# Kernel tuning notes

Hardware: AMD Instinct MI355X
Metric: run time of the kernel (lower is better)

Reference implementation:

```python
import jax, jax.numpy as jnp
import numpy as np

N, CS, CZ, H, C, PQ, PV, N0, N1 = 768, 384, 128, 12, 64, 4, 8, 192, 64
CZ4 = CZ // 4
INF, EPS = 1e5, 1e-8


def setup_inputs() -> dict:
    key = jax.random.key(0)
    ks = jax.random.split(key, 24)

    def w(k, i, o):
        return jax.random.normal(k, (i, o), jnp.float32) / np.float32(np.sqrt(i))

    s = jax.random.normal(ks[0], (N, CS), jnp.float32)
    z = jax.random.normal(ks[1], (N, N, CZ), jnp.float32)
    rot = jnp.linalg.qr(jax.random.normal(ks[2], (N, 3, 3), jnp.float32))[0]
    trans = jax.random.normal(ks[3], (N, 3), jnp.float32)
    mask = jnp.ones((N,), jnp.float32)
    is_atom = jax.random.bernoulli(ks[4], 0.5, (N,))
    return dict(
        s=s, z=z, rot=rot, trans=trans, mask=mask, is_atom=is_atom,
        wq=w(ks[5], CS, H * C), bq=jnp.zeros((H * C,), jnp.float32),
        wkv=w(ks[6], CS, 2 * H * C), bkv=jnp.zeros((2 * H * C,), jnp.float32),
        wqp=w(ks[7], CS, 3 * H * PQ), bqp=jnp.zeros((3 * H * PQ,), jnp.float32),
        wkvp=w(ks[8], CS, 3 * H * (PQ + PV)), bkvp=jnp.zeros((3 * H * (PQ + PV),), jnp.float32),
        wb=w(ks[9], CZ, H), bb=jnp.zeros((H,), jnp.float32),
        wdz=w(ks[10], CZ, CZ4), bdz=jnp.zeros((CZ4,), jnp.float32),
        head_weights=jnp.full((H,), 0.5413248, jnp.float32),  # softplus^-1(1), per ipa_point_weights_init_
        wout=w(ks[11], H * (C + 4 * PV + CZ4), CS), bout=jnp.zeros((CS,), jnp.float32),
        tfnq_ws=w(ks[12], N0, H * C), tfnq_wv=w(ks[13], N1, H * PQ),
        tfnkv_ws=w(ks[14], N0, 2 * H * C), tfnkv_wv=w(ks[15], N1, H * (PQ + PV)),
        tfno_ws=w(ks[16], H * (C + PV + CZ4), N0), tfno_wv=w(ks[17], H * PV, N1),
    )


def reference(s, z, rot, trans, mask, is_atom, wq, bq, wkv, bkv, wqp, bqp, wkvp, bkvp,
              wb, bb, wdz, bdz, head_weights, wout, bout,
              tfnq_ws, tfnq_wv, tfnkv_ws, tfnkv_wv, tfno_ws, tfno_wv):
    n = s.shape[0]

    def apply_rigid(pts):  # pts: [n, P, 3] -> R x + t
        return jnp.einsum('nij,npj->npi', rot, pts) + trans[:, None, :]

    # ---- residue (frame) path ----
    q_r = (s @ wq + bq).reshape(n, H, C)
    kv_r = (s @ wkv + bkv).reshape(n, H, 2 * C)
    k_r, v_r = kv_r[..., :C], kv_r[..., C:]
    # torch.split-in-3 then stack(dim=-1) layout: [n, 3, H*P] -> [n, H*P, 3]
    qp = (s @ wqp + bqp).reshape(n, 3, H * PQ).transpose(0, 2, 1)
    q_pts_r = apply_rigid(qp).reshape(n, H, PQ, 3)
    kvp = (s @ wkvp + bkvp).reshape(n, 3, H * (PQ + PV)).transpose(0, 2, 1)
    kv_pts_r = apply_rigid(kvp).reshape(n, H, PQ + PV, 3)
    k_pts_r, v_pts_r = kv_pts_r[..., :PQ, :], kv_pts_r[..., PQ:, :]

    # ---- atom (TFN-equivariant) path: irreps = N0 scalars + N1 vectors ----
    sc = s[:, :N0]
    vec = s[:, N0:N0 + 3 * N1].reshape(n, N1, 3)
    q_a = (sc @ tfnq_ws).reshape(n, H, C)
    q_pts_a = jnp.einsum('nix,io->nox', vec, tfnq_wv).reshape(n, H, PQ, 3) + trans[:, None, None, :]
    kv_a = (sc @ tfnkv_ws).reshape(n, H, 2 * C)
    k_a, v_a = kv_a[..., :C], kv_a[..., C:]
    kv_pts_a = jnp.einsum('nix,io->nox', vec, tfnkv_wv).reshape(n, H, PQ + PV, 3) + trans[:, None, None, :]
    k_pts_a, v_pts_a = kv_pts_a[..., :PQ, :], kv_pts_a[..., PQ:, :]

    m1 = is_atom[:, None, None]
    m2 = is_atom[:, None, None, None]
    q = jnp.where(m1, q_a, q_r)
    k = jnp.where(m1, k_a, k_r)
    v = jnp.where(m1, v_a, v_r)
    q_pts = jnp.where(m2, q_pts_a, q_pts_r)
    k_pts = jnp.where(m2, k_pts_a, k_pts_r)
    v_pts = jnp.where(m2, v_pts_a, v_pts_r)

    # ---- attention logits ----
    b = z @ wb + bb  # [n, n, H]
    a = jnp.einsum('nhc,mhc->hnm', q, k) * np.float32(np.sqrt(1.0 / (3 * C)))
    a = a + np.float32(np.sqrt(1.0 / 3)) * b.transpose(2, 0, 1)

    disp = q_pts[:, None] - k_pts[None]          # [n, n, H, PQ, 3]
    pt_att = jnp.sum(disp * disp, axis=-1)       # [n, n, H, PQ]
    hw = jax.nn.softplus(head_weights) * np.float32(np.sqrt(1.0 / (3 * (PQ * 9.0 / 2))))
    pt_att = -0.5 * jnp.sum(pt_att * hw[:, None], axis=-1)  # [n, n, H]
    a = a + pt_att.transpose(2, 0, 1)

    sq_mask = INF * (mask[:, None] * mask[None, :] - 1.0)
    a = jax.nn.softmax(a + sq_mask[None], axis=-1)  # [H, n, n]

    # ---- aggregation ----
    o = jnp.einsum('hnm,mhc->nhc', a, v).reshape(n, H * C)
    o_pt = jnp.einsum('hnm,mhpx->nhpx', a, v_pts)  # [n, H, PV, 3]
    o_pt = jnp.einsum('nji,nhpj->nhpi', rot, o_pt - trans[:, None, None, :])  # invert_apply
    o_pt_norm = jnp.sqrt(jnp.sum(o_pt * o_pt, axis=-1) + EPS).reshape(n, H * PV)
    o_pt = o_pt.reshape(n, H * PV, 3)
    pair_z = z @ wdz + bdz  # [n, n, CZ4]
    o_pair = jnp.einsum('hnm,nmz->nhz', a, pair_z).reshape(n, H * CZ4)

    # ---- residue output head ----
    res_feats = jnp.concatenate([o, o_pt[..., 0], o_pt[..., 1], o_pt[..., 2], o_pt_norm, o_pair], axis=-1)
    res_out = res_feats @ wout + bout  # [n, CS]

    # ---- atom output head (equivariant linear: scalars mix, vectors mix per-component) ----
    atom_sc = jnp.concatenate([o, o_pt_norm, o_pair], axis=-1) @ tfno_ws  # [n, N0]
    atom_vec = jnp.einsum('npx,po->nox', o_pt, tfno_wv).reshape(n, 3 * N1)
    atom_out = jnp.concatenate([atom_sc, atom_vec], axis=-1)  # [n, CS]

    return jnp.where(is_atom[:, None], atom_out, res_out)
```

## Files before the change

### kernel.cpp

```cpp
#include <hip/hip_runtime.h>
#include <hip/hip_bf16.h>

static constexpr int NN = 768;

typedef short v8bf __attribute__((ext_vector_type(8)));
typedef float v4f  __attribute__((ext_vector_type(4)));

__device__ __forceinline__ unsigned short f2bf(float f) {
  unsigned u = __float_as_uint(f);
  u += 0x7fffu + ((u >> 16) & 1u);
  return (unsigned short)(u >> 16);
}
__device__ __forceinline__ float bf2f(unsigned short s) {
  return __uint_as_float(((unsigned)s) << 16);
}

static constexpr size_t OFF_ISA    = 0;
static constexpr size_t OFF_WCT    = 1024;
static constexpr size_t OFF_BCAT   = 4096;
static constexpr size_t OFF_SBF    = 4160;
static constexpr size_t OFF_WQT    = 151616;
static constexpr size_t OFF_WKVT   = 299072;
static constexpr size_t OFF_WQPT   = 593984;
static constexpr size_t OFF_WKVPT  = 630848;
static constexpr size_t OFF_TFNQT  = 716864;
static constexpr size_t OFF_TFNKVT = 815168;
static constexpr size_t OFF_WOUTT  = 1011776;
static constexpr size_t OFF_TFNOT  = 1306688;
static constexpr size_t OFF_QR     = 1429568;
static constexpr size_t OFF_KVR    = 1724480;
static constexpr size_t OFF_QP     = 2314304;
static constexpr size_t OFF_KVP    = 2424896;
static constexpr size_t OFF_QA     = 2756672;
static constexpr size_t OFF_KVA    = 3051584;
static constexpr size_t OFF_QCAT   = 3641408;
static constexpr size_t OFF_KCAT   = 4083776;
static constexpr size_t OFF_RQ     = 4526144;
static constexpr size_t OFF_RK     = 4535360;
static constexpr size_t OFF_VCATT  = 4986944;
static constexpr size_t OFF_BB     = 5429312;
static constexpr size_t OFF_PZT    = 8968256;
static constexpr size_t OFF_ABF    = 18405440;
static constexpr size_t OFF_OPTRAW = 21944384;
static constexpr size_t OFF_RESF   = 22165568;
static constexpr size_t OFF_ATOMF  = 22755392;

__device__ void transpose_cv(const float* __restrict__ src, unsigned short* __restrict__ dst,
                             int K, int Kp, int N, int ky, int nx) {
  __shared__ float tl[32][33];
  const int k0 = ky * 32, n0 = nx * 32;
  const int tx = threadIdx.x & 31, ty = threadIdx.x >> 5;
  for (int it = 0; it < 4; ++it) {
    int r = ty + it * 8;
    float v = 0.f;
    if (k0 + r < K && n0 + tx < N) v = src[(long long)(k0 + r) * N + n0 + tx];
    tl[r][tx] = v;
  }
  __syncthreads();
  for (int it = 0; it < 4; ++it) {
    int r = ty + it * 8;
    if (n0 + r < N && k0 + tx < Kp)
      dst[(long long)(n0 + r) * Kp + k0 + tx] = f2bf(tl[tx][r]);
  }
}

__global__ __launch_bounds__(256) void prep0(
    float* wsf, const float* s, const float* wq, const float* wkv,
    const float* wqp, const float* wkvp, const float* tfnq_ws,
    const float* tfnkv_ws, const float* wout, const float* tfno_ws,
    const float* wb, const float* wdz, const float* bb, const float* bdz,
    const unsigned int* isa_raw)
{
  const int bx = blockIdx.x, t = threadIdx.x;
  if (bx < 288)       { int g = bx;        transpose_cv(wq,      (unsigned short*)(wsf+OFF_WQT),    384, 384, 768,  g/24, g%24); return; }
  else if (bx < 864)  { int g = bx-288;    transpose_cv(wkv,     (unsigned short*)(wsf+OFF_WKVT),   384, 384, 1536, g/48, g%48); return; }
  else if (bx < 924)  { int g = bx-864;    transpose_cv(wqp,     (unsigned short*)(wsf+OFF_WQPT),   384, 384, 144,  g/5,  g%5);  return; }
  else if (bx < 1092) { int g = bx-924;    transpose_cv(wkvp,    (unsigned short*)(wsf+OFF_WKVPT),  384, 384, 432,  g/14, g%14); return; }
  else if (bx < 1284) { int g = bx-1092;   transpose_cv(tfnq_ws, (unsigned short*)(wsf+OFF_TFNQT),  192, 256, 768,  g/24, g%24); return; }
  else if (bx < 1668) { int g = bx-1284;   transpose_cv(tfnkv_ws,(unsigned short*)(wsf+OFF_TFNKVT), 192, 256, 1536, g/48, g%48); return; }
  else if (bx < 2244) { int g = bx-1668;   transpose_cv(wout,    (unsigned short*)(wsf+OFF_WOUTT),  1536,1536,384,  g/12, g%12); return; }
  else if (bx < 2484) { int g = bx-2244;   transpose_cv(tfno_ws, (unsigned short*)(wsf+OFF_TFNOT),  1248,1280,192,  g/6,  g%6);  return; }
  else if (bx < 2772) {
    long long base = (long long)(bx - 2484) * 1024 + t * 4;
    float4 v = *(const float4*)(s + base);
    unsigned short tmp[4] = {f2bf(v.x), f2bf(v.y), f2bf(v.z), f2bf(v.w)};
    *(uint2*)((unsigned short*)(wsf + OFF_SBF) + base) = *(uint2*)tmp;
    return;
  } else if (bx < 2773) {
    __shared__ int notint, notfloat;
    int* ISA = (int*)(wsf + OFF_ISA);
    if (t == 0) { notint = 0; notfloat = 0; }
    __syncthreads();
    if (t < 192) {
      unsigned v = isa_raw[t];
      if (v > 1u) atomicOr(&notint, 1);
      if (v != 0u && v != 0x3F800000u) atomicOr(&notfloat, 1);
    }
    __syncthreads();
    const int mode = (!notint) ? 0 : ((!notfloat) ? 1 : 2);
    for (int n = t; n < NN; n += 256) {
      int val;
      if (mode == 2) val = (((const unsigned char*)isa_raw)[n] != 0);
      else           val = (isa_raw[n] != 0u);
      ISA[n] = val;
    }
    return;
  } else {
    const float rs3 = 0.57735026918962576f;
    unsigned short* WCT = (unsigned short*)(wsf + OFF_WCT);
    float* bcat = wsf + OFF_BCAT;
    int idx = (bx - 2773) * 256 + t;
    if (idx < 48 * 128) {
      int o = idx >> 7, k = idx & 127;
      float v = 0.f;
      if (o < 12) v = rs3 * wb[k * 12 + o];
      else if (o < 44) v = wdz[k * 32 + (o - 12)];
      WCT[o * 128 + k] = f2bf(v);
    }
    if (bx == 2773 && t < 48)
      bcat[t] = (t < 12) ? rs3 * bb[t] : (t < 44 ? bdz[t - 12] : 0.f);
  }
}

__device__ __forceinline__ void gemm16(
    char* lds, const unsigned short* __restrict__ A, int lda,
    const unsigned short* __restrict__ BT, int ldb, int KQ,
    const float* __restrict__ bias, int mode,
    float* Cf, unsigned short* Cb, int ldc, int Nc, int colb, int row0,
    const int* __restrict__ ISA, float* outp)
{
  v4f (*PS)[4][64] = (v4f (*)[4][64])lds;
  const int t = threadIdx.x, w = t >> 6, l = t & 63, l15 = l & 15, lg = l >> 4;
  const int rowA = row0 + l15;
  v4f acc[4] = {};
  const unsigned short* ap = A + (long long)rowA * lda + lg * 8;
  const int kend = (w + 1) * KQ;
  for (int k0 = w * KQ; k0 < kend; k0 += 32) {
    v8bf av = *(const v8bf*)(ap + k0);
#pragma unroll
    for (int cf = 0; cf < 4; ++cf) {
      v8bf bv = *(const v8bf*)(BT + (long long)(colb + cf * 16 + l15) * ldb + k0 + lg * 8);
      acc[cf] = __builtin_amdgcn_mfma_f32_16x16x32_bf16(av, bv, acc[cf], 0, 0, 0);
    }
  }
#pragma unroll
  for (int cf = 0; cf < 4; ++cf) PS[w][cf][l] = acc[cf];
  __syncthreads();
  const int cf = w;
  v4f sv = PS[0][cf][l] + PS[1][cf][l] + PS[2][cf][l] + PS[3][cf][l];
  const int c = colb + cf * 16 + l15;
  if (c < Nc) {
    float bvs = bias ? bias[c] : 0.f;
#pragma unroll
    for (int i = 0; i < 4; ++i) {
      int r = row0 + lg * 4 + i;
      float v = sv[i] + bvs;
      if (mode == 0)      Cf[(long long)r * ldc + c] = v;
      else if (mode == 1) Cb[(long long)r * ldc + c] = f2bf(v);
      else if (mode == 2) { if (!ISA[r]) outp[r * 384 + c] = v; }
      else                { if ( ISA[r]) outp[r * 384 + c] = v; }
    }
  }
}

__global__ __launch_bounds__(256) void mega1(
    float* wsf, const float* __restrict__ z,
    const float* bq, const float* bkv, const float* bqp, const float* bkvp)
{
  __shared__ __align__(16) char lds[23296];
  const int t = threadIdx.x;
  if (blockIdx.x < 4608) {
    float* Sout = (float*)lds;
    const unsigned short* WCT = (const unsigned short*)(wsf + OFF_WCT);
    const float* bcat = wsf + OFF_BCAT;
    unsigned short* Bb  = (unsigned short*)(wsf + OFF_BB);
    unsigned short* PZT = (unsigned short*)(wsf + OFF_PZT);
    const long long row0 = (long long)blockIdx.x * 128;
    const int w = t >> 6, l = t & 63, l15 = l & 15, lg = l >> 4;
    v8bf bvv[4][3];
#pragma unroll
    for (int ks = 0; ks < 4; ++ks)
#pragma unroll
      for (int cf = 0; cf < 3; ++cf)
        bvv[ks][cf] = *(const v8bf*)(WCT + (cf * 16 + l15) * 128 + ks * 32 + lg * 8);
    v4f acc[2][3] = {};
#pragma unroll
    for (int rf = 0; rf < 2; ++rf) {
      const float* zrow = z + (row0 + w * 32 + rf * 16 + l15) * 128 + lg * 8;
#pragma unroll
      for (int ks = 0; ks < 4; ++ks) {
        float4 a0 = *(const float4*)(zrow + ks * 32);
        float4 a1 = *(const float4*)(zrow + ks * 32 + 4);
        unsigned short tmp[8] = {f2bf(a0.x), f2bf(a0.y), f2bf(a0.z), f2bf(a0.w),
                                 f2bf(a1.x), f2bf(a1.y), f2bf(a1.z), f2bf(a1.w)};
        v8bf av = *(const v8bf*)tmp;
#pragma unroll
        for (int cf = 0; cf < 3; ++cf)
          acc[rf][cf] = __builtin_amdgcn_mfma_f32_16x16x32_bf16(av, bvv[ks][cf], acc[rf][cf], 0, 0, 0);
      }
    }
#pragma unroll
    for (int rf = 0; rf < 2; ++rf)
#pragma unroll
      for (int cf = 0; cf < 3; ++cf) {
        int o = cf * 16 + l15;
#pragma unroll
        for (int i = 0; i < 4; ++i) {
          int m = w * 32 + rf * 16 + lg * 4 + i;
          Sout[o * 132 + m] = acc[rf][cf][i];
        }
      }
    __syncthreads();
    const int n = blockIdx.x / 6;
    const int m0 = (blockIdx.x % 6) * 128;
    for (int idx = t; idx < 44 * 8; idx += 256) {
      int o = idx >> 3, seg = idx & 7;
      float bias = bcat[o];
      unsigned short tmp[16];
#pragma unroll
      for (int j = 0; j < 16; ++j) tmp[j] = f2bf(Sout[o * 132 + seg * 16 + j] + bias);
      unsigned short* gp;
      if (o < 12) gp = Bb + ((long long)o * 768 + n) * 768 + m0 + seg * 16;
      else        gp = PZT + ((long long)n * 32 + (o - 12)) * 768 + m0 + seg * 16;
      *(uint4*)gp = *(uint4*)tmp;
      *(uint4*)(gp + 8) = *(uint4*)(tmp + 8);
    }
    return;
  }
  const int g = blockIdx.x - 4608;
  const int bt = g / 82, xt = g % 82;
  const unsigned short* SBF = (const unsigned short*)(wsf + OFF_SBF);
  const unsigned short* BT; const float* bias; int ldb, KQ, mode, ldc, Nc, colb;
  float* Cf = nullptr; unsigned short* Cb = nullptr;
  if (xt < 12)      { BT=(const unsigned short*)(wsf+OFF_WQT);    bias=bq;     ldb=384; KQ=96; Cb=(unsigned short*)(wsf+OFF_QR);  ldc=768;  Nc=768;  colb=xt*64;      mode=1; }
  else if (xt < 36) { BT=(const unsigned short*)(wsf+OFF_WKVT);   bias=bkv;    ldb=384; KQ=96; Cb=(unsigned short*)(wsf+OFF_KVR); ldc=1536; Nc=1536; colb=(xt-12)*64; mode=1; }
  else if (xt < 39) { BT=(const unsigned short*)(wsf+OFF_WQPT);   bias=bqp;    ldb=384; KQ=96; Cf=wsf+OFF_QP;                     ldc=144;  Nc=144;  colb=(xt-36)*64; mode=0; }
  else if (xt < 46) { BT=(const unsigned short*)(wsf+OFF_WKVPT);  bias=bkvp;   ldb=384; KQ=96; Cf=wsf+OFF_KVP;                    ldc=432;  Nc=432;  colb=(xt-39)*64; mode=0; }
  else if (xt < 58) { BT=(const unsigned short*)(wsf+OFF_TFNQT);  bias=nullptr;ldb=256; KQ=64; Cb=(unsigned short*)(wsf+OFF_QA);  ldc=768;  Nc=768;  colb=(xt-46)*64; mode=1; }
  else              { BT=(const unsigned short*)(wsf+OFF_TFNKVT); bias=nullptr;ldb=256; KQ=64; Cb=(unsigned short*)(wsf+OFF_KVA); ldc=1536; Nc=1536; colb=(xt-58)*64; mode=1; }
  gemm16(lds, SBF, 384, BT, ldb, KQ, bias, mode, Cf, Cb, ldc, Nc, colb, bt * 16, nullptr, nullptr);
}

__global__ __launch_bounds__(256) void prep_qkv(
    float* wsf, const float* __restrict__ s,
    const float* __restrict__ rot, const float* __restrict__ trans,
    const float* __restrict__ head_w,
    const float* __restrict__ tfnq_wv, const float* __restrict__ tfnkv_wv)
{
  const int n = blockIdx.x, t = threadIdx.x;
  const int* ISA = (const int*)(wsf + OFF_ISA);
  const unsigned short* QRb  = (const unsigned short*)(wsf + OFF_QR);
  const unsigned short* KVRb = (const unsigned short*)(wsf + OFF_KVR);
  const unsigned short* QAb  = (const unsigned short*)(wsf + OFF_QA);
  const unsigned short* KVAb = (const unsigned short*)(wsf + OFF_KVA);
  const float* QP  = wsf + OFF_QP;
  const float* KVP = wsf + OFF_KVP;
  unsigned short* Qcat = (unsigned short*)(wsf + OFF_QCAT);
  unsigned short* Kcat = (unsigned short*)(wsf + OFF_KCAT);
  unsigned short* Vt   = (unsigned short*)(wsf + OFF_VCATT);
  float* rq = wsf + OFF_RQ;
  float* rk = wsf + OFF_RK;
  const bool isa = ISA[n] != 0;
  __shared__ float R[9], T[3], shw[12], sv[192];
  __shared__ float qs[768], ks[768], vs[768], qp[144], kp[144], vp[288];
  if (t < 9) R[t] = rot[n * 9 + t];
  if (t < 3) T[t] = trans[n * 3 + t];
  if (t >= 16 && t < 28)
    shw[t - 16] = log1pf(__expf(head_w[t - 16])) * 0.13608276348795434f;
  if (isa && t >= 32 && t < 224) sv[t - 32] = s[(size_t)n * 384 + 192 + (t - 32)];
  __syncthreads();
  for (int idx = t; idx < 768; idx += 256) {
    int h = idx >> 6, c = idx & 63;
    qs[idx] = bf2f(isa ? QAb[(long long)n * 768 + idx] : QRb[(long long)n * 768 + idx]);
    ks[idx] = bf2f(isa ? KVAb[(long long)n * 1536 + h * 128 + c] : KVRb[(long long)n * 1536 + h * 128 + c]);
    vs[idx] = bf2f(isa ? KVAb[(long long)n * 1536 + h * 128 + 64 + c] : KVRb[(long long)n * 1536 + h * 128 + 64 + c]);
  }
  if (isa) {
    for (int idx = t; idx < 144; idx += 256) {
      int hp = idx / 3, x = idx % 3;
      float a = 0.f;
      for (int i = 0; i < 64; ++i) a += sv[i * 3 + x] * tfnq_wv[i * 48 + hp];
      qp[idx] = a + T[x];
    }
    for (int idx = t; idx < 432; idx += 256) {
      int o = idx / 3, x = idx % 3;
      float a = 0.f;
      for (int i = 0; i < 64; ++i) a += sv[i * 3 + x] * tfnkv_wv[i * 144 + o];
      float v = a + T[x];
      int h = o / 12, pp = o % 12;
      if (pp < 4) kp[(h * 4 + pp) * 3 + x] = v;
      else        vp[(h * 8 + (pp - 4)) * 3 + x] = v;
    }
  } else {
    for (int idx = t; idx < 144; idx += 256) {
      int hp = idx / 3, i = idx % 3;
      qp[idx] = R[i * 3 + 0] * QP[(long long)n * 144 + 0 + hp] +
                R[i * 3 + 1] * QP[(long long)n * 144 + 48 + hp] +
                R[i * 3 + 2] * QP[(long long)n * 144 + 96 + hp] + T[i];
    }
    for (int idx = t; idx < 432; idx += 256) {
      int hp = idx / 3, i = idx % 3;
      float v = R[i * 3 + 0] * KVP[(long long)n * 432 + 0 + hp] +
                R[i * 3 + 1] * KVP[(long long)n * 432 + 144 + hp] +
                R[i * 3 + 2] * KVP[(long long)n * 432 + 288 + hp] + T[i];
      int h = hp / 12, pp = hp % 12;
      if (pp < 4) kp[(h * 4 + pp) * 3 + i] = v;
      else        vp[(h * 8 + (pp - 4)) * 3 + i] = v;
    }
  }
  __syncthreads();
  const float sq = 0.07216878364870322f;
  for (int idx = t; idx < 1152; idx += 256) {
    int h = idx / 96, c = idx % 96;
    float qv = (c < 64) ? sq * qs[h * 64 + c] : ((c < 76) ? shw[h] * qp[h * 12 + (c - 64)] : 0.f);
    float kv = (c < 64) ? ks[h * 64 + c]      : ((c < 76) ? kp[h * 12 + (c - 64)] : 0.f);
    float vv = (c < 64) ? vs[h * 64 + c]      : ((c < 88) ? vp[h * 24 + (c - 64)] : 0.f);
    long long base = ((long long)n * 12 + h) * 96 + c;
    Qcat[base] = f2bf(qv);
    Kcat[base] = f2bf(kv);
    Vt[((long long)h * 96 + c) * 768 + n] = f2bf(vv);
  }
  if (t < 24) {
    int h = t >> 1, which = t & 1;
    const float* p = which ? kp : qp;
    float s2 = 0.f;
#pragma unroll
    for (int d = 0; d < 12; ++d) { float x = p[h * 12 + d]; s2 += x * x; }
    float val = 0.5f * shw[h] * s2;
    if (which) rk[h * 768 + n] = val;
    else       rq[h * 768 + n] = val;
  }
}

__global__ __launch_bounds__(256) void mega2(float* wsf, const float* __restrict__ mask) {
  __shared__ __align__(16) char lds[26112];
  const int t = threadIdx.x;
  const unsigned short* Qcat = (const unsigned short*)(wsf + OFF_QCAT);
  const unsigned short* Kcat = (const unsigned short*)(wsf + OFF_KCAT);
  const unsigned short* Bb   = (const unsigned short*)(wsf + OFF_BB);
  const unsigned short* VcatT= (const unsigned short*)(wsf + OFF_VCATT);
  const float* rq = wsf + OFF_RQ;
  const float* rk = wsf + OFF_RK;
  unsigned short* Abf   = (unsigned short*)(wsf + OFF_ABF);
  unsigned short* RESF  = (unsigned short*)(wsf + OFF_RESF);
  unsigned short* ATOMF = (unsigned short*)(wsf + OFF_ATOMF);
  float* OPTRAW = wsf + OFF_OPTRAW;
  const int h = blockIdx.x / 48, r0 = (blockIdx.x % 48) * 16;
  const int w = t >> 6, l = t & 63, l15 = l & 15, lg = l >> 4;
  unsigned short* SW = (unsigned short*)lds + w * 3200;
  float* redm = (float*)(lds + 25600);
  float* reds = (float*)(lds + 25856);
  const int nrow = r0 + l15;
  v8bf aq[3];
#pragma unroll
  for (int ks = 0; ks < 3; ++ks)
    aq[ks] = *(const v8bf*)(Qcat + ((long long)nrow * 12 + h) * 96 + ks * 32 + lg * 8);
  v4f acc[12] = {};
#pragma unroll
  for (int cf = 0; cf < 12; ++cf) {
    int m = w * 192 + cf * 16 + l15;
    const unsigned short* kb = Kcat + ((long long)m * 12 + h) * 96 + lg * 8;
#pragma unroll
    for (int ks = 0; ks < 3; ++ks) {
      v8bf bv = *(const v8bf*)(kb + ks * 32);
      acc[cf] = __builtin_amdgcn_mfma_f32_16x16x32_bf16(aq[ks], bv, acc[cf], 0, 0, 0);
    }
  }
#pragma unroll
  for (int it = 0; it < 6; ++it) {
    int chunk = it * 64 + l;
    int row = chunk / 24, cc = (chunk % 24) * 8;
    *(uint4*)(SW + row * 200 + cc) =
        *(const uint4*)(Bb + ((long long)(h * 768 + r0 + row)) * 768 + w * 192 + cc);
  }
  __syncthreads();
  float rkm[12], mkm[12];
#pragma unroll
  for (int cf = 0; cf < 12; ++cf) {
    int m = w * 192 + cf * 16 + l15;
    rkm[cf] = rk[h * 768 + m];
    mkm[cf] = mask[m];
  }
  float rqn[4], mkn[4], mymax[4];
#pragma unroll
  for (int i = 0; i < 4; ++i) {
    int gn = r0 + lg * 4 + i;
    rqn[i] = rq[h * 768 + gn];
    mkn[i] = mask[gn];
    mymax[i] = -3.0e38f;
  }
#pragma unroll
  for (int cf = 0; cf < 12; ++cf)
#pragma unroll
    for (int i = 0; i < 4; ++i) {
      float v = acc[cf][i] + bf2f(SW[(lg * 4 + i) * 200 + cf * 16 + l15])
              - rqn[i] - rkm[cf] + 100000.0f * (mkn[i] * mkm[cf] - 1.0f);
      acc[cf][i] = v;
      mymax[i] = fmaxf(mymax[i], v);
    }
#pragma unroll
  for (int off = 1; off < 16; off <<= 1)
#pragma unroll
    for (int i = 0; i < 4; ++i) mymax[i] = fmaxf(mymax[i], __shfl_xor(mymax[i], off, 64));
  if (l15 == 0) {
#pragma unroll
    for (int i = 0; i < 4; ++i) redm[w * 16 + lg * 4 + i] = mymax[i];
  }
  __syncthreads();
  float mx[4], mysum[4];
#pragma unroll
  for (int i = 0; i < 4; ++i) {
    int rl = lg * 4 + i;
    mx[i] = fmaxf(fmaxf(redm[rl], redm[16 + rl]), fmaxf(redm[32 + rl], redm[48 + rl]));
    mysum[i] = 0.f;
  }
#pragma unroll
  for (int cf = 0; cf < 12; ++cf)
#pragma unroll
    for (int i = 0; i < 4; ++i) {
      float e = __expf(acc[cf][i] - mx[i]);
      acc[cf][i] = e;
      mysum[i] += e;
    }
#pragma unroll
  for (int off = 1; off < 16; off <<= 1)
#pragma unroll
    for (int i = 0; i < 4; ++i) mysum[i] += __shfl_xor(mysum[i], off, 64);
  if (l15 == 0) {
#pragma unroll
    for (int i = 0; i < 4; ++i) reds[w * 16 + lg * 4 + i] = mysum[i];
  }
  __syncthreads();
  float inv[4];
#pragma unroll
  for (int i = 0; i < 4; ++i) {
    int rl = lg * 4 + i;
    inv[i] = 1.0f / (reds[rl] + reds[16 + rl] + reds[32 + rl] + reds[48 + rl]);
  }
#pragma unroll
  for (int cf = 0; cf < 12; ++cf)
#pragma unroll
    for (int i = 0; i < 4; ++i)
      SW[(lg * 4 + i) * 200 + cf * 16 + l15] = f2bf(acc[cf][i] * inv[i]);
  __syncthreads();
#pragma unroll
  for (int it = 0; it < 6; ++it) {
    int chunk = it * 64 + l;
    int row = chunk / 24, cc = (chunk % 24) * 8;
    *(uint4*)(Abf + ((long long)(h * 768 + r0 + row)) * 768 + w * 192 + cc) =
        *(const uint4*)(SW + row * 200 + cc);
  }
  const unsigned short* vbase = VcatT + (long long)h * 96 * 768 + w * 192 + lg * 8;
  v4f acc2[6] = {};
  for (int kk = 0; kk < 192; kk += 32) {
    v8bf av = *(const v8bf*)(SW + l15 * 200 + kk + lg * 8);
#pragma unroll
    for (int cf = 0; cf < 6; ++cf) {
      v8bf bv = *(const v8bf*)(vbase + (long long)(cf * 16 + l15) * 768 + kk);
      acc2[cf] = __builtin_amdgcn_mfma_f32_16x16x32_bf16(av, bv, acc2[cf], 0, 0, 0);
    }
  }
  __syncthreads();
  v4f (*PS)[64] = (v4f (*)[64])lds;
#pragma unroll
  for (int cf = 0; cf < 6; ++cf) PS[w * 6 + cf][l] = acc2[cf];
  __syncthreads();
  for (int cf = w; cf < 6; cf += 4) {
    v4f sv = PS[cf][l] + PS[6 + cf][l] + PS[12 + cf][l] + PS[18 + cf][l];
    int c = cf * 16 + l15;
    int rb = r0 + lg * 4;
#pragma unroll
    for (int i = 0; i < 4; ++i) {
      int n = rb + i;
      float v = sv[i];
      if (c < 64) {
        unsigned short b = f2bf(v);
        RESF[(long long)n * 1536 + h * 64 + c] = b;
        ATOMF[(long long)n * 1280 + h * 64 + c] = b;
      } else if (c < 88) {
        OPTRAW[(long long)n * 288 + h * 24 + (c - 64)] = v;
      }
    }
  }
}

__global__ __launch_bounds__(256) void mega3(
    float* wsf, const float* __restrict__ rot, const float* __restrict__ trans,
    const float* __restrict__ tfno_wv, float* __restrict__ out)
{
  const int t = threadIdx.x;
  unsigned short* RESF  = (unsigned short*)(wsf + OFF_RESF);
  unsigned short* ATOMF = (unsigned short*)(wsf + OFF_ATOMF);
  if (blockIdx.x < 768) {
    __shared__ __align__(16) v4f PS[8][64];
    const unsigned short* Abf = (const unsigned short*)(wsf + OFF_ABF);
    const unsigned short* PZT = (const unsigned short*)(wsf + OFF_PZT);
    const int w = t >> 6, l = t & 63, l15 = l & 15, lg = l >> 4;
    const int n = blockIdx.x;
    const int hh = (l15 < 12) ? l15 : 0;
    const unsigned short* arow = Abf + ((long long)hh * 768 + n) * 768 + lg * 8;
    const unsigned short* pz = PZT + (long long)n * 32 * 768 + lg * 8;
    v4f acc[2] = {};
    for (int k0 = w * 192; k0 < w * 192 + 192; k0 += 32) {
      v8bf av = *(const v8bf*)(arow + k0);
#pragma unroll
      for (int cf = 0; cf < 2; ++cf) {
        v8bf bv = *(const v8bf*)(pz + (long long)(cf * 16 + l15) * 768 + k0);
        acc[cf] = __builtin_amdgcn_mfma_f32_16x16x32_bf16(av, bv, acc[cf], 0, 0, 0);
      }
    }
    PS[w * 2 + 0][l] = acc[0];
    PS[w * 2 + 1][l] = acc[1];
    __syncthreads();
    if (t < 128) {
      int cf = t >> 6, ll = t & 63;
      v4f sv = PS[cf][ll] + PS[2 + cf][ll] + PS[4 + cf][ll] + PS[6 + cf][ll];
      int zc = cf * 16 + (ll & 15);
#pragma unroll
      for (int i = 0; i < 4; ++i) {
        int hd = (ll >> 4) * 4 + i;
        if (hd < 12) {
          unsigned short b = f2bf(sv[i]);
          RESF[(long long)n * 1536 + 1152 + hd * 32 + zc] = b;
          ATOMF[(long long)n * 1280 + 864 + hd * 32 + zc] = b;
        }
      }
    }
    return;
  }
  {
    const int n = blockIdx.x - 768;
    const float* OPTRAW = wsf + OFF_OPTRAW;
    const int* ISA = (const int*)(wsf + OFF_ISA);
    const bool isa = ISA[n] != 0;
    __shared__ float R[9], T[3], opt2[96][3], norml[96];
    if (t < 9) R[t] = rot[(size_t)n * 9 + t];
    if (t < 3) T[t] = trans[(size_t)n * 3 + t];
    __syncthreads();
    for (int idx = t; idx < 288; idx += 256) {
      int hp = idx / 3, i = idx % 3;
      float x = OPTRAW[(size_t)n * 288 + hp * 3 + 0] - T[0];
      float y = OPTRAW[(size_t)n * 288 + hp * 3 + 1] - T[1];
      float z = OPTRAW[(size_t)n * 288 + hp * 3 + 2] - T[2];
      opt2[hp][i] = R[0 + i] * x + R[3 + i] * y + R[6 + i] * z;
    }
    __syncthreads();
    if (t < 96)
      norml[t] = sqrtf(opt2[t][0] * opt2[t][0] + opt2[t][1] * opt2[t][1] +
                       opt2[t][2] * opt2[t][2] + 1e-8f);
    __syncthreads();
    const long long rb = (long long)n * 1536;
    const long long ab = (long long)n * 1280;
    for (int idx = t; idx < 288; idx += 256) {
      int x = idx / 96, hp = idx % 96;
      RESF[rb + 768 + idx] = f2bf(opt2[hp][x]);
    }
    for (int idx = t; idx < 96; idx += 256) {
      unsigned short b = f2bf(norml[idx]);
      RESF[rb + 1056 + idx] = b;
      ATOMF[ab + 768 + idx] = b;
    }
    if (isa) {
      for (int idx = t; idx < 192; idx += 256) {
        int o = idx / 3, x = idx % 3;
        float a = 0.f;
        for (int p = 0; p < 96; ++p) a += opt2[p][x] * tfno_wv[p * 64 + o];
        out[(size_t)n * 384 + 192 + idx] = a;
      }
    }
  }
}

__global__ __launch_bounds__(256) void outg(float* wsf, const float* __restrict__ bout,
                                            float* __restrict__ out) {
  __shared__ __align__(16) char lds[16384];
  const int g = blockIdx.x;
  const int bt = g / 9, xt = g % 9;
  const int* ISA = (const int*)(wsf + OFF_ISA);
  if (xt < 6)
    gemm16(lds, (const unsigned short*)(wsf + OFF_RESF), 1536,
           (const unsigned short*)(wsf + OFF_WOUTT), 1536, 384, bout, 2,
           nullptr, nullptr, 0, 384, xt * 64, bt * 16, ISA, out);
  else
    gemm16(lds, (const unsigned short*)(wsf + OFF_ATOMF), 1280,
           (const unsigned short*)(wsf + OFF_TFNOT), 1280, 320, nullptr, 3,
           nullptr, nullptr, 0, 192, (xt - 6) * 64, bt * 16, ISA, out);
}

extern "C" void kernel_launch(void* const* d_in, const int* in_sizes, int n_in,
                              void* d_out, int out_size, void* d_ws, size_t ws_size,
                              hipStream_t stream) {
  (void)in_sizes; (void)n_in; (void)out_size; (void)ws_size;
  const float* s      = (const float*)d_in[0];
  const float* z      = (const float*)d_in[1];
  const float* rot    = (const float*)d_in[2];
  const float* trans  = (const float*)d_in[3];
  const float* mask   = (const float*)d_in[4];
  const float* wq     = (const float*)d_in[6];
  const float* bq     = (const float*)d_in[7];
  const float* wkv    = (const float*)d_in[8];
  const float* bkv    = (const float*)d_in[9];
  const float* wqp    = (const float*)d_in[10];
  const float* bqp    = (const float*)d_in[11];
  const float* wkvp   = (const float*)d_in[12];
  const float* bkvp   = (const float*)d_in[13];
  const float* wb     = (const float*)d_in[14];
  const float* bb     = (const float*)d_in[15];
  const float* wdz    = (const float*)d_in[16];
  const float* bdz    = (const float*)d_in[17];
  const float* head_w = (const float*)d_in[18];
  const float* wout   = (const float*)d_in[19];
  const float* bout   = (const float*)d_in[20];
  const float* tfnq_ws  = (const float*)d_in[21];
  const float* tfnq_wv  = (const float*)d_in[22];
  const float* tfnkv_ws = (const float*)d_in[23];
  const float* tfnkv_wv = (const float*)d_in[24];
  const float* tfno_ws  = (const float*)d_in[25];
  const float* tfno_wv  = (const float*)d_in[26];

  float* wsf = (float*)d_ws;

  prep0<<<2797, 256, 0, stream>>>(wsf, s, wq, wkv, wqp, wkvp, tfnq_ws, tfnkv_ws,
                                  wout, tfno_ws, wb, wdz, bb, bdz,
                                  (const unsigned int*)d_in[5]);
  mega1<<<8544, 256, 0, stream>>>(wsf, z, bq, bkv, bqp, bkvp);
  prep_qkv<<<768, 256, 0, stream>>>(wsf, s, rot, trans, head_w, tfnq_wv, tfnkv_wv);
  mega2<<<576, 256, 0, stream>>>(wsf, mask);
  mega3<<<1536, 256, 0, stream>>>(wsf, rot, trans, tfno_wv, (float*)d_out);
  outg<<<432, 256, 0, stream>>>(wsf, bout, (float*)d_out);
}
```

Measured before the change: 186.1 us.

## Widen attention kernel to 8 waves, move output-weight transposes into mega1

The attention kernel mega2 now runs 512 threads per block, with each wave covering 96 key columns instead of 192. This halves the per-wave register accumulators and adds more parallelism, at the cost of twice the LDS and an 8-way cross-wave reduction. The attention-probability buffer is stored in [n][h][m] layout, so mega3 reads the 12 heads for a row from contiguous memory. The wout and tfno_ws transposes move out of prep0 into extra blocks of mega1, shortening the prep kernel and overlapping that work with the z projection.

```diff
diff --git a/kernel.cpp b/kernel.cpp
--- a/kernel.cpp
+++ b/kernel.cpp
@@ -45,11 +45,12 @@
 static constexpr size_t OFF_RESF   = 22165568;
 static constexpr size_t OFF_ATOMF  = 22755392;
 
-__device__ void transpose_cv(const float* __restrict__ src, unsigned short* __restrict__ dst,
+__device__ void transpose_cv(char* ldsbuf, const float* __restrict__ src,
+                             unsigned short* __restrict__ dst,
                              int K, int Kp, int N, int ky, int nx) {
-  __shared__ float tl[32][33];
+  float (*tl)[33] = (float (*)[33])ldsbuf;
   const int k0 = ky * 32, n0 = nx * 32;
-  const int tx = threadIdx.x & 31, ty = threadIdx.x >> 5;
+  const int tx = threadIdx.x & 31, ty = (threadIdx.x & 255) >> 5;
   for (int it = 0; it < 4; ++it) {
     int r = ty + it * 8;
     float v = 0.f;
@@ -67,26 +68,24 @@
 __global__ __launch_bounds__(256) void prep0(
     float* wsf, const float* s, const float* wq, const float* wkv,
     const float* wqp, const float* wkvp, const float* tfnq_ws,
-    const float* tfnkv_ws, const float* wout, const float* tfno_ws,
-    const float* wb, const float* wdz, const float* bb, const float* bdz,
-    const unsigned int* isa_raw)
+    const float* tfnkv_ws, const float* wb, const float* wdz,
+    const float* bb, const float* bdz, const unsigned int* isa_raw)
 {
+  __shared__ __align__(16) char lds[4224];
   const int bx = blockIdx.x, t = threadIdx.x;
-  if (bx < 288)       { int g = bx;        transpose_cv(wq,      (unsigned short*)(wsf+OFF_WQT),    384, 384, 768,  g/24, g%24); return; }
-  else if (bx < 864)  { int g = bx-288;    transpose_cv(wkv,     (unsigned short*)(wsf+OFF_WKVT),   384, 384, 1536, g/48, g%48); return; }
-  else if (bx < 924)  { int g = bx-864;    transpose_cv(wqp,     (unsigned short*)(wsf+OFF_WQPT),   384, 384, 144,  g/5,  g%5);  return; }
-  else if (bx < 1092) { int g = bx-924;    transpose_cv(wkvp,    (unsigned short*)(wsf+OFF_WKVPT),  384, 384, 432,  g/14, g%14); return; }
-  else if (bx < 1284) { int g = bx-1092;   transpose_cv(tfnq_ws, (unsigned short*)(wsf+OFF_TFNQT),  192, 256, 768,  g/24, g%24); return; }
-  else if (bx < 1668) { int g = bx-1284;   transpose_cv(tfnkv_ws,(unsigned short*)(wsf+OFF_TFNKVT), 192, 256, 1536, g/48, g%48); return; }
-  else if (bx < 2244) { int g = bx-1668;   transpose_cv(wout,    (unsigned short*)(wsf+OFF_WOUTT),  1536,1536,384,  g/12, g%12); return; }
-  else if (bx < 2484) { int g = bx-2244;   transpose_cv(tfno_ws, (unsigned short*)(wsf+OFF_TFNOT),  1248,1280,192,  g/6,  g%6);  return; }
-  else if (bx < 2772) {
-    long long base = (long long)(bx - 2484) * 1024 + t * 4;
+  if (bx < 288)       { int g = bx;        transpose_cv(lds, wq,      (unsigned short*)(wsf+OFF_WQT),    384, 384, 768,  g/24, g%24); return; }
+  else if (bx < 864)  { int g = bx-288;    transpose_cv(lds, wkv,     (unsigned short*)(wsf+OFF_WKVT),   384, 384, 1536, g/48, g%48); return; }
+  else if (bx < 924)  { int g = bx-864;    transpose_cv(lds, wqp,     (unsigned short*)(wsf+OFF_WQPT),   384, 384, 144,  g/5,  g%5);  return; }
+  else if (bx < 1092) { int g = bx-924;    transpose_cv(lds, wkvp,    (unsigned short*)(wsf+OFF_WKVPT),  384, 384, 432,  g/14, g%14); return; }
+  else if (bx < 1284) { int g = bx-1092;   transpose_cv(lds, tfnq_ws, (unsigned short*)(wsf+OFF_TFNQT),  192, 256, 768,  g/24, g%24); return; }
+  else if (bx < 1668) { int g = bx-1284;   transpose_cv(lds, tfnkv_ws,(unsigned short*)(wsf+OFF_TFNKVT), 192, 256, 1536, g/48, g%48); return; }
+  else if (bx < 1956) {
+    long long base = (long long)(bx - 1668) * 1024 + t * 4;
     float4 v = *(const float4*)(s + base);
     unsigned short tmp[4] = {f2bf(v.x), f2bf(v.y), f2bf(v.z), f2bf(v.w)};
     *(uint2*)((unsigned short*)(wsf + OFF_SBF) + base) = *(uint2*)tmp;
     return;
-  } else if (bx < 2773) {
+  } else if (bx < 1957) {
     __shared__ int notint, notfloat;
     int* ISA = (int*)(wsf + OFF_ISA);
     if (t == 0) { notint = 0; notfloat = 0; }
@@ -109,7 +108,7 @@
     const float rs3 = 0.57735026918962576f;
     unsigned short* WCT = (unsigned short*)(wsf + OFF_WCT);
     float* bcat = wsf + OFF_BCAT;
-    int idx = (bx - 2773) * 256 + t;
+    int idx = (bx - 1957) * 256 + t;
     if (idx < 48 * 128) {
       int o = idx >> 7, k = idx & 127;
       float v = 0.f;
@@ -117,7 +116,7 @@
       else if (o < 44) v = wdz[k * 32 + (o - 12)];
       WCT[o * 128 + k] = f2bf(v);
     }
-    if (bx == 2773 && t < 48)
+    if (bx == 1957 && t < 48)
       bcat[t] = (t < 12) ? rs3 * bb[t] : (t < 44 ? bdz[t - 12] : 0.f);
   }
 }
@@ -165,7 +164,8 @@
 
 __global__ __launch_bounds__(256) void mega1(
     float* wsf, const float* __restrict__ z,
-    const float* bq, const float* bkv, const float* bqp, const float* bkvp)
+    const float* bq, const float* bkv, const float* bqp, const float* bkvp,
+    const float* wout, const float* tfno_ws)
 {
   __shared__ __align__(16) char lds[23296];
   const int t = threadIdx.x;
@@ -225,6 +225,12 @@
       *(uint4*)gp = *(uint4*)tmp;
       *(uint4*)(gp + 8) = *(uint4*)(tmp + 8);
     }
+    return;
+  }
+  if (blockIdx.x >= 8544) {
+    const int g = blockIdx.x - 8544;
+    if (g < 576) transpose_cv(lds, wout,    (unsigned short*)(wsf+OFF_WOUTT), 1536, 1536, 384, g/12, g%12);
+    else         transpose_cv(lds, tfno_ws, (unsigned short*)(wsf+OFF_TFNOT), 1248, 1280, 192, (g-576)/6, (g-576)%6);
     return;
   }
   const int g = blockIdx.x - 4608;
@@ -332,8 +338,8 @@
   }
 }
 
-__global__ __launch_bounds__(256) void mega2(float* wsf, const float* __restrict__ mask) {
-  __shared__ __align__(16) char lds[26112];
+__global__ __launch_bounds__(512) void mega2(float* wsf, const float* __restrict__ mask) {
+  __shared__ __align__(16) char lds[50176];
   const int t = threadIdx.x;
   const unsigned short* Qcat = (const unsigned short*)(wsf + OFF_QCAT);
   const unsigned short* Kcat = (const unsigned short*)(wsf + OFF_KCAT);
@@ -341,24 +347,24 @@
   const unsigned short* VcatT= (const unsigned short*)(wsf + OFF_VCATT);
   const float* rq = wsf + OFF_RQ;
   const float* rk = wsf + OFF_RK;
-  unsigned short* Abf   = (unsigned short*)(wsf + OFF_ABF);
+  unsigned short* Abf2  = (unsigned short*)(wsf + OFF_ABF);
   unsigned short* RESF  = (unsigned short*)(wsf + OFF_RESF);
   unsigned short* ATOMF = (unsigned short*)(wsf + OFF_ATOMF);
   float* OPTRAW = wsf + OFF_OPTRAW;
   const int h = blockIdx.x / 48, r0 = (blockIdx.x % 48) * 16;
   const int w = t >> 6, l = t & 63, l15 = l & 15, lg = l >> 4;
-  unsigned short* SW = (unsigned short*)lds + w * 3200;
-  float* redm = (float*)(lds + 25600);
-  float* reds = (float*)(lds + 25856);
+  unsigned short* SW = (unsigned short*)(lds + w * 3328);
+  float* redm = (float*)(lds + 49152);
+  float* reds = (float*)(lds + 49664);
   const int nrow = r0 + l15;
   v8bf aq[3];
 #pragma unroll
   for (int ks = 0; ks < 3; ++ks)
     aq[ks] = *(const v8bf*)(Qcat + ((long long)nrow * 12 + h) * 96 + ks * 32 + lg * 8);
-  v4f acc[12] = {};
-#pragma unroll
-  for (int cf = 0; cf < 12; ++cf) {
-    int m = w * 192 + cf * 16 + l15;
+  v4f acc[6] = {};
+#pragma unroll
+  for (int cf = 0; cf < 6; ++cf) {
+    int m = w * 96 + cf * 16 + l15;
     const unsigned short* kb = Kcat + ((long long)m * 12 + h) * 96 + lg * 8;
 #pragma unroll
     for (int ks = 0; ks < 3; ++ks) {
@@ -367,17 +373,17 @@
     }
   }
 #pragma unroll
-  for (int it = 0; it < 6; ++it) {
+  for (int it = 0; it < 3; ++it) {
     int chunk = it * 64 + l;
-    int row = chunk / 24, cc = (chunk % 24) * 8;
-    *(uint4*)(SW + row * 200 + cc) =
-        *(const uint4*)(Bb + ((long long)(h * 768 + r0 + row)) * 768 + w * 192 + cc);
-  }
-  __syncthreads();
-  float rkm[12], mkm[12];
-#pragma unroll
-  for (int cf = 0; cf < 12; ++cf) {
-    int m = w * 192 + cf * 16 + l15;
+    int row = chunk / 12, cc = (chunk % 12) * 8;
+    *(uint4*)(SW + row * 104 + cc) =
+        *(const uint4*)(Bb + ((long long)(h * 768 + r0 + row)) * 768 + w * 96 + cc);
+  }
+  __syncthreads();
+  float rkm[6], mkm[6];
+#pragma unroll
+  for (int cf = 0; cf < 6; ++cf) {
+    int m = w * 96 + cf * 16 + l15;
     rkm[cf] = rk[h * 768 + m];
     mkm[cf] = mask[m];
   }
@@ -390,10 +396,10 @@
     mymax[i] = -3.0e38f;
   }
 #pragma unroll
-  for (int cf = 0; cf < 12; ++cf)
+  for (int cf = 0; cf < 6; ++cf)
 #pragma unroll
     for (int i = 0; i < 4; ++i) {
-      float v = acc[cf][i] + bf2f(SW[(lg * 4 + i) * 200 + cf * 16 + l15])
+      float v = acc[cf][i] + bf2f(SW[(lg * 4 + i) * 104 + cf * 16 + l15])
               - rqn[i] - rkm[cf] + 100000.0f * (mkn[i] * mkm[cf] - 1.0f);
       acc[cf][i] = v;
       mymax[i] = fmaxf(mymax[i], v);
@@ -411,11 +417,15 @@
 #pragma unroll
   for (int i = 0; i < 4; ++i) {
     int rl = lg * 4 + i;
-    mx[i] = fmaxf(fmaxf(redm[rl], redm[16 + rl]), fmaxf(redm[32 + rl], redm[48 + rl]));
+    float m0 = fmaxf(redm[rl], redm[16 + rl]);
+    float m1 = fmaxf(redm[32 + rl], redm[48 + rl]);
+    float m2 = fmaxf(redm[64 + rl], redm[80 + rl]);
+    float m3 = fmaxf(redm[96 + rl], redm[112 + rl]);
+    mx[i] = fmaxf(fmaxf(m0, m1), fmaxf(m2, m3));
     mysum[i] = 0.f;
   }
 #pragma unroll
-  for (int cf = 0; cf < 12; ++cf)
+  for (int cf = 0; cf < 6; ++cf)
 #pragma unroll
     for (int i = 0; i < 4; ++i) {
       float e = __expf(acc[cf][i] - mx[i]);
@@ -435,25 +445,27 @@
 #pragma unroll
   for (int i = 0; i < 4; ++i) {
     int rl = lg * 4 + i;
-    inv[i] = 1.0f / (reds[rl] + reds[16 + rl] + reds[32 + rl] + reds[48 + rl]);
-  }
-#pragma unroll
-  for (int cf = 0; cf < 12; ++cf)
+    float s0 = reds[rl] + reds[16 + rl] + reds[32 + rl] + reds[48 + rl];
+    float s1 = reds[64 + rl] + reds[80 + rl] + reds[96 + rl] + reds[112 + rl];
+    inv[i] = 1.0f / (s0 + s1);
+  }
+#pragma unroll
+  for (int cf = 0; cf < 6; ++cf)
 #pragma unroll
     for (int i = 0; i < 4; ++i)
-      SW[(lg * 4 + i) * 200 + cf * 16 + l15] = f2bf(acc[cf][i] * inv[i]);
-  __syncthreads();
-#pragma unroll
-  for (int it = 0; it < 6; ++it) {
+      SW[(lg * 4 + i) * 104 + cf * 16 + l15] = f2bf(acc[cf][i] * inv[i]);
+#pragma unroll
+  for (int it = 0; it < 3; ++it) {
     int chunk = it * 64 + l;
-    int row = chunk / 24, cc = (chunk % 24) * 8;
-    *(uint4*)(Abf + ((long long)(h * 768 + r0 + row)) * 768 + w * 192 + cc) =
-        *(const uint4*)(SW + row * 200 + cc);
-  }
-  const unsigned short* vbase = VcatT + (long long)h * 96 * 768 + w * 192 + lg * 8;
+    int row = chunk / 12, cc = (chunk % 12) * 8;
+    *(uint4*)(Abf2 + ((long long)(r0 + row) * 12 + h) * 768 + w * 96 + cc) =
+        *(const uint4*)(SW + row * 104 + cc);
+  }
+  const unsigned short* vbase = VcatT + (long long)h * 96 * 768 + w * 96 + lg * 8;
   v4f acc2[6] = {};
-  for (int kk = 0; kk < 192; kk += 32) {
-    v8bf av = *(const v8bf*)(SW + l15 * 200 + kk + lg * 8);
+#pragma unroll
+  for (int kk = 0; kk < 96; kk += 32) {
+    v8bf av = *(const v8bf*)(SW + l15 * 104 + kk + lg * 8);
 #pragma unroll
     for (int cf = 0; cf < 6; ++cf) {
       v8bf bv = *(const v8bf*)(vbase + (long long)(cf * 16 + l15) * 768 + kk);
@@ -465,10 +477,13 @@
 #pragma unroll
   for (int cf = 0; cf < 6; ++cf) PS[w * 6 + cf][l] = acc2[cf];
   __syncthreads();
-  for (int cf = w; cf < 6; cf += 4) {
-    v4f sv = PS[cf][l] + PS[6 + cf][l] + PS[12 + cf][l] + PS[18 + cf][l];
-    int c = cf * 16 + l15;
-    int rb = r0 + lg * 4;
+  if (t < 384) {
+    int cf = t >> 6, ll = t & 63;
+    v4f sv = PS[cf][ll];
+#pragma unroll
+    for (int ww = 1; ww < 8; ++ww) sv += PS[ww * 6 + cf][ll];
+    int c = cf * 16 + (ll & 15);
+    int rb = r0 + (ll >> 4) * 4;
 #pragma unroll
     for (int i = 0; i < 4; ++i) {
       int n = rb + i;
@@ -493,12 +508,12 @@
   unsigned short* ATOMF = (unsigned short*)(wsf + OFF_ATOMF);
   if (blockIdx.x < 768) {
     __shared__ __align__(16) v4f PS[8][64];
-    const unsigned short* Abf = (const unsigned short*)(wsf + OFF_ABF);
+    const unsigned short* Abf2 = (const unsigned short*)(wsf + OFF_ABF);
     const unsigned short* PZT = (const unsigned short*)(wsf + OFF_PZT);
     const int w = t >> 6, l = t & 63, l15 = l & 15, lg = l >> 4;
     const int n = blockIdx.x;
     const int hh = (l15 < 12) ? l15 : 0;
-    const unsigned short* arow = Abf + ((long long)hh * 768 + n) * 768 + lg * 8;
+    const unsigned short* arow = Abf2 + ((long long)n * 12 + hh) * 768 + lg * 8;
     const unsigned short* pz = PZT + (long long)n * 32 * 768 + lg * 8;
     v4f acc[2] = {};
     for (int k0 = w * 192; k0 < w * 192 + 192; k0 += 32) {
@@ -620,12 +635,11 @@
 
   float* wsf = (float*)d_ws;
 
-  prep0<<<2797, 256, 0, stream>>>(wsf, s, wq, wkv, wqp, wkvp, tfnq_ws, tfnkv_ws,
-                                  wout, tfno_ws, wb, wdz, bb, bdz,
-                                  (const unsigned int*)d_in[5]);
-  mega1<<<8544, 256, 0, stream>>>(wsf, z, bq, bkv, bqp, bkvp);
+  prep0<<<1981, 256, 0, stream>>>(wsf, s, wq, wkv, wqp, wkvp, tfnq_ws, tfnkv_ws,
+                                  wb, wdz, bb, bdz, (const unsigned int*)d_in[5]);
+  mega1<<<9360, 256, 0, stream>>>(wsf, z, bq, bkv, bqp, bkvp, wout, tfno_ws);
   prep_qkv<<<768, 256, 0, stream>>>(wsf, s, rot, trans, head_w, tfnq_wv, tfnkv_wv);
-  mega2<<<576, 256, 0, stream>>>(wsf, mask);
+  mega2<<<576, 512, 0, stream>>>(wsf, mask);
   mega3<<<1536, 256, 0, stream>>>(wsf, rot, trans, tfno_wv, (float*)d_out);
   outg<<<432, 256, 0, stream>>>(wsf, bout, (float*)d_out);
 }
```

Result: no change. 187.0 us (+0.5%).
